# Performance work log

Hardware: AMD Instinct MI355X
Metric: run time of the kernel (lower is better)

## Reference

```python
import jax, jax.numpy as jnp
import numpy as np

NA, NT, NG = 100000, 300000, 2000        # artist / track / genre node counts
EPT, ETG = 600000, 400000                # performed / has_genre edge counts
IN_A, IN_T, IN_G = 64, 96, 32            # raw feature dims per node type
HID, HEADS, OUT, L = 64, 4, 64, 2        # GATv2 per-head dim = HID, concat=False
NEG_SLOPE = 0.2                          # GATv2 LeakyReLU slope


def setup_inputs() -> dict:
    key = jax.random.key(0)
    ks = jax.random.split(key, 32)
    f = lambda k, s, sc: jax.random.normal(k, s, dtype=jnp.float32) * sc
    z = lambda s: jnp.zeros(s, dtype=jnp.float32)
    return {
        "x_artist": f(ks[0], (NA, IN_A), 1.0),
        "x_track": f(ks[1], (NT, IN_T), 1.0),
        "x_genre": f(ks[2], (NG, IN_G), 1.0),
        "enc_Wa": f(ks[3], (IN_A, HID), 0.05), "enc_ba": z((HID,)),
        "enc_Wt": f(ks[4], (IN_T, HID), 0.05), "enc_bt": z((HID,)),
        "enc_Wg": f(ks[5], (IN_G, HID), 0.05), "enc_bg": z((HID,)),
        "src_pt": jax.random.randint(ks[6], (EPT,), 0, NA, dtype=jnp.int32),
        "dst_pt": jax.random.randint(ks[7], (EPT,), 0, NT, dtype=jnp.int32),
        "src_tg": jax.random.randint(ks[8], (ETG,), 0, NT, dtype=jnp.int32),
        "dst_tg": jax.random.randint(ks[9], (ETG,), 0, NG, dtype=jnp.int32),
        "Wl_pt": f(ks[10], (L, HID, HEADS, HID), 0.05), "bl_pt": z((L, HEADS, HID)),
        "Wr_pt": f(ks[11], (L, HID, HEADS, HID), 0.05), "br_pt": z((L, HEADS, HID)),
        "att_pt": f(ks[12], (L, HEADS, HID), 0.05), "bias_pt": z((L, HID)),
        "Wl_tg": f(ks[13], (L, HID, HEADS, HID), 0.05), "bl_tg": z((L, HEADS, HID)),
        "Wr_tg": f(ks[14], (L, HID, HEADS, HID), 0.05), "br_tg": z((L, HEADS, HID)),
        "att_tg": f(ks[15], (L, HEADS, HID), 0.05), "bias_tg": z((L, HID)),
        "lin_track_W": f(ks[16], (HID, OUT), 0.05), "lin_track_b": z((OUT,)),
        "lin_genre_W": f(ks[17], (HID, OUT), 0.05), "lin_genre_b": z((OUT,)),
    }


def _gatv2(xs, xd, src, dst, Wl, bl, Wr, br, att, bias, n_dst):
    """Bipartite GATv2Conv, heads averaged (concat=False), no self loops, eval mode."""
    gl = jnp.einsum("nd,dhc->nhc", xs, Wl) + bl            # [Ns,H,C] src transform
    gr = jnp.einsum("nd,dhc->nhc", xd, Wr) + br            # [Nd,H,C] dst transform
    e = jax.nn.leaky_relu(gl[src] + gr[dst], NEG_SLOPE)    # [E,H,C]
    s = jnp.einsum("ehc,hc->eh", e, att)                   # [E,H] logits
    m = jax.ops.segment_max(s, dst, num_segments=n_dst)    # per-dst softmax (stable)
    m = jnp.where(jnp.isfinite(m), m, 0.0)
    ex = jnp.exp(s - m[dst])
    den = jax.ops.segment_sum(ex, dst, num_segments=n_dst)
    alpha = ex / (den[dst] + 1e-16)                        # [E,H]
    out = jax.ops.segment_sum(gl[src] * alpha[:, :, None], dst, num_segments=n_dst)
    return out.mean(axis=1) + bias                         # [Nd,C]


def _l2norm(x):
    n = jnp.sqrt(jnp.sum(x * x, axis=-1, keepdims=True))
    return x / jnp.maximum(n, 1e-12)


def reference(x_artist, x_track, x_genre, enc_Wa, enc_ba, enc_Wt, enc_bt, enc_Wg, enc_bg,
              src_pt, dst_pt, src_tg, dst_tg,
              Wl_pt, bl_pt, Wr_pt, br_pt, att_pt, bias_pt,
              Wl_tg, bl_tg, Wr_tg, br_tg, att_tg, bias_tg,
              lin_track_W, lin_track_b, lin_genre_W, lin_genre_b):
    enc_a = x_artist @ enc_Wa + enc_ba
    enc_t = x_track @ enc_Wt + enc_bt
    enc_g = x_genre @ enc_Wg + enc_bg
    # Faithful to source: every layer reads the encoder output (hidden never fed back),
    # so only the last layer's weights determine the result.
    for l in range(L):
        h_track = jax.nn.elu(_gatv2(enc_a, enc_t, src_pt, dst_pt,
                                    Wl_pt[l], bl_pt[l], Wr_pt[l], br_pt[l],
                                    att_pt[l], bias_pt[l], NT))
        h_genre = jax.nn.elu(_gatv2(enc_t, enc_g, src_tg, dst_tg,
                                    Wl_tg[l], bl_tg[l], Wr_tg[l], br_tg[l],
                                    att_tg[l], bias_tg[l], NG))
    out_track = _l2norm(h_track @ lin_track_W + lin_track_b)
    out_genre = _l2norm(h_genre @ lin_genre_W + lin_genre_b)
    return out_track, out_genre
```

## Files before the change

kernel.cpp:

```cpp
#include <hip/hip_runtime.h>
#include <hip/hip_bf16.h>

typedef __hip_bfloat16 bf16;
typedef __attribute__((ext_vector_type(8))) short short8;
typedef __attribute__((ext_vector_type(4))) float f32x4;

#define NA 100000
#define NT 300000
#define NG 2000
#define EPT 600000
#define ETG 400000

#define DSB 64
#define DBK 64

#define DPP_QX1 0xB1
#define DPP_QX2 0x4E
#define DPP_RR4 0x124
#define DPP_RR8 0x128

template <int CTRL>
__device__ __forceinline__ float dppadd(float x) {
    int y = __builtin_amdgcn_update_dpp(0, __float_as_int(x), CTRL, 0xf, 0xf, true);
    return x + __int_as_float(y);
}

__device__ __forceinline__ float b2f(short s) {
    return __uint_as_float(((unsigned)(unsigned short)s) << 16);
}
__device__ __forceinline__ void cvt16(short8 a, short8 b, float* f) {
#pragma unroll
    for (int j = 0; j < 8; ++j) f[j] = b2f(a[j]);
#pragma unroll
    for (int j = 0; j < 8; ++j) f[8 + j] = b2f(b[j]);
}
__device__ __forceinline__ short f2bs(float x) {
    return (short)__builtin_bit_cast(unsigned short, __float2bfloat16(x));
}

__global__ void fill_u32(unsigned* __restrict__ p, unsigned v, long n) {
    long i = (long)blockIdx.x * 256 + threadIdx.x;
    if (i < n) p[i] = v;
}

__global__ __launch_bounds__(256) void wprep(
    const float* __restrict__ We, const float* __restrict__ Wl,
    const float* __restrict__ bl, const float* __restrict__ be,
    short* __restrict__ Bf, float* __restrict__ bc, int KS)
{
    int t = blockIdx.x * 256 + threadIdx.x;
    if (t < KS * 1024) {
        int c = t & 15, kb = (t >> 4) & 3, nt = (t >> 6) & 15, ks = t >> 10;
        int k0 = ks * 32 + kb * 8, n = nt * 16 + c;
        short8 o;
#pragma unroll
        for (int j = 0; j < 8; ++j) {
            int k = k0 + j;
            float acc = 0.f;
            for (int cc = 0; cc < 64; ++cc)
                acc = fmaf(We[k * 64 + cc], Wl[cc * 256 + n], acc);
            o[j] = f2bs(acc);
        }
        ((short8*)Bf)[t] = o;
    }
    if (blockIdx.x == 0) {
        int j = threadIdx.x;
        float acc = bl[j];
        for (int cc = 0; cc < 64; ++cc) acc = fmaf(be[cc], Wl[cc * 256 + j], acc);
        bc[j] = acc;
    }
}

template <int KS>
__global__ __launch_bounds__(256) void tformf(
    const float* __restrict__ A, const short* __restrict__ Bf,
    const float* __restrict__ bias, bf16* __restrict__ C, int M)
{
    constexpr int K = KS * 32;
    int wv = threadIdx.x >> 6, lane = threadIdx.x & 63;
    int lrow = lane & 15, kb = lane >> 4;
    int base = blockIdx.x * 64 + wv * 16;

    int arow = base + lrow; if (arow >= M) arow = M - 1;
    const float* Ap = A + (size_t)arow * K + kb * 8;
    short8 a[KS];
#pragma unroll
    for (int s = 0; s < KS; ++s) {
        f32x4 lo = *(const f32x4*)(Ap + s * 32);
        f32x4 hi = *(const f32x4*)(Ap + s * 32 + 4);
#pragma unroll
        for (int j = 0; j < 4; ++j) {
            a[s][j]     = f2bs(lo[j]);
            a[s][4 + j] = f2bs(hi[j]);
        }
    }

    const short8* Bl = (const short8*)Bf + kb * 16 + lrow;

    f32x4 acc[16];
#pragma unroll
    for (int nt = 0; nt < 16; ++nt) {
        float bv = bias[nt * 16 + lrow];
        f32x4 bvv = {bv, bv, bv, bv};
        acc[nt] = bvv;
    }
#pragma unroll
    for (int nt = 0; nt < 16; ++nt) {
#pragma unroll
        for (int s = 0; s < KS; ++s)
            acc[nt] = __builtin_amdgcn_mfma_f32_16x16x32_bf16(
                a[s], Bl[(s * 16 + nt) * 64], acc[nt], 0, 0, 0);
    }
    int r0 = base + kb * 4;
#pragma unroll
    for (int nt = 0; nt < 16; ++nt) {
#pragma unroll
        for (int r = 0; r < 4; ++r) {
            int row = r0 + r;
            if (row < M)
                C[(size_t)row * 256 + nt * 16 + lrow] = __float2bfloat16(acc[nt][r]);
        }
    }
}

__global__ __launch_bounds__(256) void histo(
    const int* __restrict__ dst, unsigned* __restrict__ cnt, int base, int E)
{
    int i = blockIdx.x * 256 + threadIdx.x;
    if (i < E) atomicAdd(&cnt[base + dst[i]], 1u);
}

__global__ __launch_bounds__(256) void scan_a(
    const unsigned* __restrict__ in, unsigned* __restrict__ out,
    unsigned* __restrict__ part, int n)
{
    __shared__ unsigned ts[256];
    int t = threadIdx.x;
    long base = (long)blockIdx.x * 1024 + (long)t * 4;
    unsigned v0 = 0, v1 = 0, v2 = 0, v3 = 0;
    if (base + 0 < n) v0 = in[base + 0];
    if (base + 1 < n) v1 = in[base + 1];
    if (base + 2 < n) v2 = in[base + 2];
    if (base + 3 < n) v3 = in[base + 3];
    unsigned s = v0 + v1 + v2 + v3;
    ts[t] = s;
    __syncthreads();
    unsigned run = s;
    for (int off = 1; off < 256; off <<= 1) {
        unsigned y = (t >= off) ? ts[t - off] : 0u;
        __syncthreads();
        run += y; ts[t] = run;
        __syncthreads();
    }
    unsigned ex = run - s;
    if (base + 0 < n) out[base + 0] = ex;
    if (base + 1 < n) out[base + 1] = ex + v0;
    if (base + 2 < n) out[base + 2] = ex + v0 + v1;
    if (base + 3 < n) out[base + 3] = ex + v0 + v1 + v2;
    if (t == 255) part[blockIdx.x] = run;
}

__global__ __launch_bounds__(256) void scan_c(
    unsigned* __restrict__ rp, const unsigned* __restrict__ part,
    unsigned* __restrict__ cur, int n)
{
    long i = (long)blockIdx.x * 256 + threadIdx.x;
    if (i >= n) return;
    unsigned v = rp[i] + part[i >> 10];
    rp[i] = v;
    if (i < n - 1) cur[i] = v;
}

__global__ __launch_bounds__(256) void scat(
    const int* __restrict__ src, const int* __restrict__ dst,
    unsigned* __restrict__ cur, int base, int* __restrict__ ss, int E)
{
    int i = blockIdx.x * 256 + threadIdx.x;
    if (i < E) {
        unsigned p = atomicAdd(&cur[base + dst[i]], 1u);
        ss[p] = src[i];
    }
}

__global__ __launch_bounds__(256) void deg_cnt(
    const unsigned* __restrict__ rp, unsigned* __restrict__ bcnt, int n)
{
    __shared__ unsigned hcnt[DBK];
    int b = blockIdx.x;
    int chunk = (n + DSB - 1) / DSB;
    int lo = b * chunk, hi = min(n, lo + chunk);
    if (threadIdx.x < DBK) hcnt[threadIdx.x] = 0u;
    __syncthreads();
    for (int i = lo + threadIdx.x; i < hi; i += 256) {
        unsigned deg = rp[i + 1] - rp[i];
        if (deg > DBK - 1) deg = DBK - 1;
        atomicAdd(&hcnt[deg], 1u);
    }
    __syncthreads();
    if (threadIdx.x < DBK) bcnt[(size_t)threadIdx.x * DSB + b] = hcnt[threadIdx.x];
}

__global__ __launch_bounds__(256) void scan4k(
    const unsigned* __restrict__ in, unsigned* __restrict__ out)
{
    __shared__ unsigned ts[256];
    int t = threadIdx.x;
    unsigned v[16]; unsigned s = 0;
#pragma unroll
    for (int j = 0; j < 16; ++j) { v[j] = in[t * 16 + j]; s += v[j]; }
    ts[t] = s;
    __syncthreads();
    unsigned run = s;
    for (int off = 1; off < 256; off <<= 1) {
        unsigned y = (t >= off) ? ts[t - off] : 0u;
        __syncthreads();
        run += y; ts[t] = run;
        __syncthreads();
    }
    unsigned ex = run - s;
#pragma unroll
    for (int j = 0; j < 16; ++j) { out[t * 16 + j] = ex; ex += v[j]; }
}

__global__ __launch_bounds__(256) void deg_place(
    const unsigned* __restrict__ rp, const unsigned* __restrict__ base,
    int* __restrict__ order, int n)
{
    __shared__ unsigned hcur[DBK];
    int b = blockIdx.x;
    int chunk = (n + DSB - 1) / DSB;
    int lo = b * chunk, hi = min(n, lo + chunk);
    if (threadIdx.x < DBK) hcur[threadIdx.x] = base[(size_t)threadIdx.x * DSB + b];
    __syncthreads();
    for (int i = lo + threadIdx.x; i < hi; i += 256) {
        unsigned deg = rp[i + 1] - rp[i];
        if (deg > DBK - 1) deg = DBK - 1;
        unsigned p = atomicAdd(&hcur[deg], 1u);
        order[p] = i;
    }
}

__global__ __launch_bounds__(256) void gat_w(
    const bf16* __restrict__ gl, const bf16* __restrict__ gr,
    const int* __restrict__ ssrc, const unsigned* __restrict__ rp,
    const int* __restrict__ order,
    const float* __restrict__ att, const float* __restrict__ bias,
    const float* __restrict__ linW, const float* __restrict__ linb,
    float* __restrict__ outp, int Nd)
{
    __shared__ float WL[4096];
    __shared__ float bL[64];
    __shared__ float hC[64];
    __shared__ float hL[16][68];
    for (int t = threadIdx.x; t < 4096; t += 256) WL[t] = linW[t];
    if (threadIdx.x < 64) {
        float b = bias[threadIdx.x];
        bL[threadIdx.x] = b;
        hC[threadIdx.x] = b > 0.f ? b : (__expf(b) - 1.f);
    }
    __syncthreads();

    int grp = threadIdx.x >> 4, g = threadIdx.x & 15;
    int h = g & 3, q = g >> 2;
    int eoff = h * 64 + q * 16;

    float at[16];
#pragma unroll
    for (int j = 0; j < 16; ++j) at[j] = att[eoff + j];
    f32x4 lbv = *(const f32x4*)(linb + g * 4);

    f32x4 ycn;
    {
        float y0 = lbv[0], y1 = lbv[1], y2 = lbv[2], y3 = lbv[3];
#pragma unroll
        for (int c = 0; c < 64; c += 4) {
            f32x4 hv = *(const f32x4*)&hC[c];
            const float* wr = WL + c * 64 + g * 4;
            f32x4 w0 = *(const f32x4*)(wr);
            f32x4 w1 = *(const f32x4*)(wr + 64);
            f32x4 w2 = *(const f32x4*)(wr + 128);
            f32x4 w3 = *(const f32x4*)(wr + 192);
            y0 = fmaf(hv[0], w0[0], y0); y1 = fmaf(hv[0], w0[1], y1);
            y2 = fmaf(hv[0], w0[2], y2); y3 = fmaf(hv[0], w0[3], y3);
            y0 = fmaf(hv[1], w1[0], y0); y1 = fmaf(hv[1], w1[1], y1);
            y2 = fmaf(hv[1], w1[2], y2); y3 = fmaf(hv[1], w1[3], y3);
            y0 = fmaf(hv[2], w2[0], y0); y1 = fmaf(hv[2], w2[1], y1);
            y2 = fmaf(hv[2], w2[2], y2); y3 = fmaf(hv[2], w2[3], y3);
            y0 = fmaf(hv[3], w3[0], y0); y1 = fmaf(hv[3], w3[1], y1);
            y2 = fmaf(hv[3], w3[2], y2); y3 = fmaf(hv[3], w3[3], y3);
        }
        float ss = y0 * y0 + y1 * y1 + y2 * y2 + y3 * y3;
        ss = dppadd<DPP_QX1>(ss);
        ss = dppadd<DPP_QX2>(ss);
        ss = dppadd<DPP_RR4>(ss);
        ss = dppadd<DPP_RR8>(ss);
        float rn = 1.f / fmaxf(sqrtf(ss), 1e-12f);
        ycn[0] = y0 * rn; ycn[1] = y1 * rn; ycn[2] = y2 * rn; ycn[3] = y3 * rn;
    }

    long ngroups = (Nd + 15) >> 4;
    for (long it = blockIdx.x; it < ngroups; it += gridDim.x) {
        long idx = it * 16 + grp;
        if (idx >= Nd) continue;
        int d = order[idx];
        unsigned beg = rp[d], end = rp[d + 1];
        if (beg == end) {
            *(f32x4*)(outp + (size_t)d * 64 + g * 4) = ycn;
            continue;
        }
        const short* grow = (const short*)gr + (size_t)d * 256 + eoff;
        short8 gr0 = *(const short8*)grow;
        short8 gr1 = *(const short8*)(grow + 8);
        float grf[16];
        cvt16(gr0, gr1, grf);

        float den = 0.f;
        float acc[16];
#pragma unroll
        for (int j = 0; j < 16; ++j) acc[j] = 0.f;

        unsigned e = beg;
        {
            int si = ssrc[e];
            const short* p0 = (const short*)gl + (size_t)si * 256 + eoff;
            short8 gA = *(const short8*)p0;
            short8 gB = *(const short8*)(p0 + 8);
            while (true) {
                float glf[16];
                cvt16(gA, gB, glf);
                ++e;
                bool more = e < end;
                if (more) {
                    int s2 = ssrc[e];
                    const short* p2 = (const short*)gl + (size_t)s2 * 256 + eoff;
                    gA = *(const short8*)p2;
                    gB = *(const short8*)(p2 + 8);
                }
                float pd = 0.f;
#pragma unroll
                for (int j = 0; j < 16; ++j) {
                    float v = glf[j] + grf[j];
                    float lr = fmaxf(v, 0.2f * v);
                    pd = fmaf(lr, at[j], pd);
                }
                pd = dppadd<DPP_RR4>(pd);
                pd = dppadd<DPP_RR8>(pd);
                float w = __expf(pd);
                den += w;
#pragma unroll
                for (int j = 0; j < 16; ++j) acc[j] = fmaf(w, glf[j], acc[j]);
                if (!more) break;
            }
        }
        float inv = 1.f / den;

        float x[16];
#pragma unroll
        for (int j = 0; j < 16; ++j) {
            float v = acc[j] * inv;
            v = dppadd<DPP_QX1>(v);
            v = dppadd<DPP_QX2>(v);
            x[j] = v;
        }
#pragma unroll
        for (int j = 0; j < 16; ++j) {
            float v = fmaf(0.25f, x[j], bL[q * 16 + j]);
            x[j] = v > 0.f ? v : (__expf(v) - 1.f);
        }
        if (h == 0) {
#pragma unroll
            for (int j = 0; j < 16; ++j) hL[grp][q * 16 + j] = x[j];
        }
        __builtin_amdgcn_wave_barrier();

        float y0 = lbv[0], y1 = lbv[1], y2 = lbv[2], y3 = lbv[3];
#pragma unroll
        for (int c = 0; c < 64; c += 4) {
            f32x4 hv = *(const f32x4*)&hL[grp][c];
            const float* wr = WL + c * 64 + g * 4;
            f32x4 w0 = *(const f32x4*)(wr);
            f32x4 w1 = *(const f32x4*)(wr + 64);
            f32x4 w2 = *(const f32x4*)(wr + 128);
            f32x4 w3 = *(const f32x4*)(wr + 192);
            y0 = fmaf(hv[0], w0[0], y0); y1 = fmaf(hv[0], w0[1], y1);
            y2 = fmaf(hv[0], w0[2], y2); y3 = fmaf(hv[0], w0[3], y3);
            y0 = fmaf(hv[1], w1[0], y0); y1 = fmaf(hv[1], w1[1], y1);
            y2 = fmaf(hv[1], w1[2], y2); y3 = fmaf(hv[1], w1[3], y3);
            y0 = fmaf(hv[2], w2[0], y0); y1 = fmaf(hv[2], w2[1], y1);
            y2 = fmaf(hv[2], w2[2], y2); y3 = fmaf(hv[2], w2[3], y3);
            y0 = fmaf(hv[3], w3[0], y0); y1 = fmaf(hv[3], w3[1], y1);
            y2 = fmaf(hv[3], w3[2], y2); y3 = fmaf(hv[3], w3[3], y3);
        }
        float ss = y0 * y0 + y1 * y1 + y2 * y2 + y3 * y3;
        ss = dppadd<DPP_QX1>(ss);
        ss = dppadd<DPP_QX2>(ss);
        ss = dppadd<DPP_RR4>(ss);
        ss = dppadd<DPP_RR8>(ss);
        float rn = 1.f / fmaxf(sqrtf(ss), 1e-12f);
        f32x4 yo = {y0 * rn, y1 * rn, y2 * rn, y3 * rn};
        *(f32x4*)(outp + (size_t)d * 64 + g * 4) = yo;
    }
}

__global__ __launch_bounds__(256) void gat_b(
    const bf16* __restrict__ gl, const bf16* __restrict__ gr,
    const int* __restrict__ ssrc, const unsigned* __restrict__ rp,
    const float* __restrict__ att, const float* __restrict__ bias,
    const float* __restrict__ linW, const float* __restrict__ linb,
    float* __restrict__ outp, int Nd)
{
    __shared__ float accL[16][256];
    __shared__ float denL[16][4];
    int grp = threadIdx.x >> 4, g = threadIdx.x & 15;
    int h = g & 3, q = g >> 2;
    int eoff = h * 64 + q * 16;
    int d = blockIdx.x;

    float at[16];
#pragma unroll
    for (int j = 0; j < 16; ++j) at[j] = att[eoff + j];

    const short* grow = (const short*)gr + (size_t)d * 256 + eoff;
    short8 gr0 = *(const short8*)grow;
    short8 gr1 = *(const short8*)(grow + 8);
    float grf[16];
    cvt16(gr0, gr1, grf);

    unsigned beg = rp[d], end = rp[d + 1];
    float den = 0.f;
    float acc[16];
#pragma unroll
    for (int j = 0; j < 16; ++j) acc[j] = 0.f;

    unsigned e = beg + grp;
    if (e < end) {
        int si = ssrc[e];
        const short* p0 = (const short*)gl + (size_t)si * 256 + eoff;
        short8 gA = *(const short8*)p0;
        short8 gB = *(const short8*)(p0 + 8);
        while (true) {
            float glf[16];
            cvt16(gA, gB, glf);
            e += 16;
            bool more = e < end;
            if (more) {
                int s2 = ssrc[e];
                const short* p2 = (const short*)gl + (size_t)s2 * 256 + eoff;
                gA = *(const short8*)p2;
                gB = *(const short8*)(p2 + 8);
            }
            float pd = 0.f;
#pragma unroll
            for (int j = 0; j < 16; ++j) {
                float v = glf[j] + grf[j];
                float lr = fmaxf(v, 0.2f * v);
                pd = fmaf(lr, at[j], pd);
            }
            pd = dppadd<DPP_RR4>(pd);
            pd = dppadd<DPP_RR8>(pd);
            float w = __expf(pd);
            den += w;
#pragma unroll
            for (int j = 0; j < 16; ++j) acc[j] = fmaf(w, glf[j], acc[j]);
            if (!more) break;
        }
    }
#pragma unroll
    for (int j = 0; j < 16; ++j) accL[grp][eoff + j] = acc[j];
    if (q == 0) denL[grp][h] = den;
    __syncthreads();

    int t = threadIdx.x;
    int hh = t >> 6, cc = t & 63;
    float sa = 0.f, sd = 0.f;
#pragma unroll
    for (int k = 0; k < 16; ++k) { sa += accL[k][hh * 64 + cc]; sd += denL[k][hh]; }
    float xv = sd > 0.f ? sa / sd : 0.f;
    __syncthreads();
    accL[0][t] = xv;
    __syncthreads();
    if (t < 64) {
        float m4 = 0.25f * (accL[0][t] + accL[0][64 + t] + accL[0][128 + t] + accL[0][192 + t]);
        float v = m4 + bias[t];
        accL[1][t] = v > 0.f ? v : (__expf(v) - 1.f);
    }
    __syncthreads();
    if (t < 64) {
        float y = linb[t];
        for (int c = 0; c < 64; ++c) y = fmaf(accL[1][c], linW[c * 64 + t], y);
        float ss = y * y;
        ss += __shfl_xor(ss, 1);  ss += __shfl_xor(ss, 2);  ss += __shfl_xor(ss, 4);
        ss += __shfl_xor(ss, 8);  ss += __shfl_xor(ss, 16); ss += __shfl_xor(ss, 32);
        float rn = 1.f / fmaxf(sqrtf(ss), 1e-12f);
        outp[(size_t)d * 64 + t] = y * rn;
    }
}


static inline unsigned gridFor(long n) { return (unsigned)((n + 255) / 256); }

extern "C" void kernel_launch(void* const* d_in, const int* in_sizes, int n_in,
                              void* d_out, int out_size, void* d_ws, size_t ws_size,
                              hipStream_t stream) {
    const float* x_artist = (const float*)d_in[0];
    const float* x_track  = (const float*)d_in[1];
    const float* x_genre  = (const float*)d_in[2];
    const float* enc_Wa = (const float*)d_in[3];  const float* enc_ba = (const float*)d_in[4];
    const float* enc_Wt = (const float*)d_in[5];  const float* enc_bt = (const float*)d_in[6];
    const float* enc_Wg = (const float*)d_in[7];  const float* enc_bg = (const float*)d_in[8];
    const int* src_pt = (const int*)d_in[9];
    const int* dst_pt = (const int*)d_in[10];
    const int* src_tg = (const int*)d_in[11];
    const int* dst_tg = (const int*)d_in[12];
    const float* Wl_pt   = (const float*)d_in[13] + 64 * 256;
    const float* bl_pt   = (const float*)d_in[14] + 256;
    const float* Wr_pt   = (const float*)d_in[15] + 64 * 256;
    const float* br_pt   = (const float*)d_in[16] + 256;
    const float* att_pt  = (const float*)d_in[17] + 256;
    const float* bias_pt = (const float*)d_in[18] + 64;
    const float* Wl_tg   = (const float*)d_in[19] + 64 * 256;
    const float* bl_tg   = (const float*)d_in[20] + 256;
    const float* Wr_tg   = (const float*)d_in[21] + 64 * 256;
    const float* br_tg   = (const float*)d_in[22] + 256;
    const float* att_tg  = (const float*)d_in[23] + 256;
    const float* bias_tg = (const float*)d_in[24] + 64;
    const float* lin_track_W = (const float*)d_in[25];
    const float* lin_track_b = (const float*)d_in[26];
    const float* lin_genre_W = (const float*)d_in[27];
    const float* lin_genre_b = (const float*)d_in[28];

    float* out = (float*)d_out;

    const int NTOT = NT + NG;

    char* p = (char*)d_ws;
    auto take = [&](size_t bytes) { char* q = p; p += (bytes + 255) & ~(size_t)255; return q; };
    char* region = take((size_t)NA * 256 * 2 + (size_t)NT * 256 * 2);
    bf16*  gl_pt  = (bf16*)region;
    bf16*  gr_pt  = (bf16*)(region + (size_t)NA * 256 * 2);
    bf16*  gl_tg  = (bf16*)region;
    unsigned* counts = (unsigned*)take((size_t)(NTOT + 1) * 4);
    unsigned* rowptr = (unsigned*)take((size_t)(NTOT + 1) * 4);
    unsigned* cursor = (unsigned*)take((size_t)NTOT * 4);
    unsigned* part   = (unsigned*)take((size_t)2048 * 4);
    int*      ssrc   = (int*)take((size_t)(EPT + ETG) * 4);
    int*      order  = (int*)take((size_t)NT * 4);
    unsigned* bcnt   = (unsigned*)take((size_t)DBK * DSB * 4);
    unsigned* bbase  = (unsigned*)take((size_t)DBK * DSB * 4);
    bf16*     gr_tg  = (bf16*)take((size_t)NG * 256 * 2);
    short*    Bf     = (short*)take((size_t)(64 + 96 + 96 + 32) * 256 * 2);
    float*    bc     = (float*)take((size_t)4 * 256 * 4);

    short* BfGLpt = Bf;
    short* BfGRpt = BfGLpt + 64 * 256;
    short* BfGLtg = BfGRpt + 96 * 256;
    short* BfGRtg = BfGLtg + 96 * 256;
    float* bcGLpt = bc;
    float* bcGRpt = bc + 256;
    float* bcGLtg = bc + 512;
    float* bcGRtg = bc + 768;

    dim3 blk(256);

    wprep<<<8,  blk, 0, stream>>>(enc_Wa, Wl_pt, bl_pt, enc_ba, BfGLpt, bcGLpt, 2);
    wprep<<<12, blk, 0, stream>>>(enc_Wt, Wr_pt, br_pt, enc_bt, BfGRpt, bcGRpt, 3);
    wprep<<<12, blk, 0, stream>>>(enc_Wt, Wl_tg, bl_tg, enc_bt, BfGLtg, bcGLtg, 3);
    wprep<<<4,  blk, 0, stream>>>(enc_Wg, Wr_tg, br_tg, enc_bg, BfGRtg, bcGRtg, 1);

    {
        int n = NTOT + 1;
        unsigned sgrid = (unsigned)((n + 1023) / 1024);
        fill_u32<<<gridFor(n), blk, 0, stream>>>(counts, 0u, n);
        histo<<<gridFor(EPT), blk, 0, stream>>>(dst_pt, counts, 0, EPT);
        histo<<<gridFor(ETG), blk, 0, stream>>>(dst_tg, counts, NT, ETG);
        scan_a<<<sgrid, blk, 0, stream>>>(counts, rowptr, part, n);
        scan_a<<<1, blk, 0, stream>>>(part, part, part + 1536, (int)sgrid);
        scan_c<<<gridFor(n), blk, 0, stream>>>(rowptr, part, cursor, n);
        scat<<<gridFor(EPT), blk, 0, stream>>>(src_pt, dst_pt, cursor, 0, ssrc, EPT);
        scat<<<gridFor(ETG), blk, 0, stream>>>(src_tg, dst_tg, cursor, NT, ssrc, ETG);
    }

    deg_cnt  <<<DSB, blk, 0, stream>>>(rowptr, bcnt, NT);
    scan4k   <<<1,   blk, 0, stream>>>(bcnt, bbase);
    deg_place<<<DSB, blk, 0, stream>>>(rowptr, bbase, order, NT);

    tformf<2><<<(NA + 63) / 64, blk, 0, stream>>>(x_artist, BfGLpt, bcGLpt, gl_pt, NA);
    tformf<3><<<(NT + 63) / 64, blk, 0, stream>>>(x_track,  BfGRpt, bcGRpt, gr_pt, NT);

    gat_w<<<2048, blk, 0, stream>>>(gl_pt, gr_pt, ssrc, rowptr, order, att_pt, bias_pt,
                                    lin_track_W, lin_track_b, out, NT);

    tformf<3><<<(NT + 63) / 64, blk, 0, stream>>>(x_track, BfGLtg, bcGLtg, gl_tg, NT);
    tformf<1><<<(NG + 63) / 64, blk, 0, stream>>>(x_genre, BfGRtg, bcGRtg, gr_tg, NG);

    gat_b<<<NG, blk, 0, stream>>>(gl_tg, gr_tg, ssrc, rowptr + NT, att_tg, bias_tg,
                                  lin_genre_W, lin_genre_b, out + (size_t)NT * 64, NG);
}
```

Measured before the change: 864.0 us.

## Permute GEMM output columns for vector stores and unroll edge loop by two

The weight-prep and bias indexing are permuted so that each lane holds 16 contiguous output columns. The GEMM epilogue can then pack bf16 pairs and write two 16-byte vector stores per row instead of 64 scalar 2-byte stores. The per-destination edge aggregation loop is rewritten to handle one odd edge and then process edges two at a time with independent gathers, which exposes more memory-level parallelism than the earlier one-ahead prefetch. The cost is higher register pressure, and the correctness of the column permutation depends on how the consumers interpret the layout.

```diff
diff --git a/kernel.cpp b/kernel.cpp
--- a/kernel.cpp
+++ b/kernel.cpp
@@ -4,6 +4,7 @@
 typedef __hip_bfloat16 bf16;
 typedef __attribute__((ext_vector_type(8))) short short8;
 typedef __attribute__((ext_vector_type(4))) float f32x4;
+typedef __attribute__((ext_vector_type(4))) unsigned u32x4;
 
 #define NA 100000
 #define NT 300000
@@ -51,7 +52,7 @@
     int t = blockIdx.x * 256 + threadIdx.x;
     if (t < KS * 1024) {
         int c = t & 15, kb = (t >> 4) & 3, nt = (t >> 6) & 15, ks = t >> 10;
-        int k0 = ks * 32 + kb * 8, n = nt * 16 + c;
+        int k0 = ks * 32 + kb * 8, n = c * 16 + nt;
         short8 o;
 #pragma unroll
         for (int j = 0; j < 8; ++j) {
@@ -100,7 +101,7 @@
     f32x4 acc[16];
 #pragma unroll
     for (int nt = 0; nt < 16; ++nt) {
-        float bv = bias[nt * 16 + lrow];
+        float bv = bias[lrow * 16 + nt];
         f32x4 bvv = {bv, bv, bv, bv};
         acc[nt] = bvv;
     }
@@ -113,13 +114,21 @@
     }
     int r0 = base + kb * 4;
 #pragma unroll
-    for (int nt = 0; nt < 16; ++nt) {
-#pragma unroll
-        for (int r = 0; r < 4; ++r) {
-            int row = r0 + r;
-            if (row < M)
-                C[(size_t)row * 256 + nt * 16 + lrow] = __float2bfloat16(acc[nt][r]);
-        }
+    for (int r = 0; r < 4; ++r) {
+        int row = r0 + r;
+        if (row >= M) continue;
+        unsigned w[8];
+#pragma unroll
+        for (int n4 = 0; n4 < 8; ++n4) {
+            unsigned lo = (unsigned)(unsigned short)f2bs(acc[2 * n4][r]);
+            unsigned hi = (unsigned)(unsigned short)f2bs(acc[2 * n4 + 1][r]);
+            w[n4] = lo | (hi << 16);
+        }
+        u32x4 v0 = {w[0], w[1], w[2], w[3]};
+        u32x4 v1 = {w[4], w[5], w[6], w[7]};
+        u32x4* dst = (u32x4*)(C + (size_t)row * 256 + lrow * 16);
+        dst[0] = v0;
+        dst[1] = v1;
     }
 }
 
@@ -320,37 +329,55 @@
         for (int j = 0; j < 16; ++j) acc[j] = 0.f;
 
         unsigned e = beg;
-        {
+        if ((end - beg) & 1u) {
             int si = ssrc[e];
             const short* p0 = (const short*)gl + (size_t)si * 256 + eoff;
             short8 gA = *(const short8*)p0;
             short8 gB = *(const short8*)(p0 + 8);
-            while (true) {
-                float glf[16];
-                cvt16(gA, gB, glf);
-                ++e;
-                bool more = e < end;
-                if (more) {
-                    int s2 = ssrc[e];
-                    const short* p2 = (const short*)gl + (size_t)s2 * 256 + eoff;
-                    gA = *(const short8*)p2;
-                    gB = *(const short8*)(p2 + 8);
-                }
-                float pd = 0.f;
-#pragma unroll
-                for (int j = 0; j < 16; ++j) {
-                    float v = glf[j] + grf[j];
-                    float lr = fmaxf(v, 0.2f * v);
-                    pd = fmaf(lr, at[j], pd);
-                }
-                pd = dppadd<DPP_RR4>(pd);
-                pd = dppadd<DPP_RR8>(pd);
-                float w = __expf(pd);
-                den += w;
-#pragma unroll
-                for (int j = 0; j < 16; ++j) acc[j] = fmaf(w, glf[j], acc[j]);
-                if (!more) break;
+            float glf[16];
+            cvt16(gA, gB, glf);
+            float pd = 0.f;
+#pragma unroll
+            for (int j = 0; j < 16; ++j) {
+                float v = glf[j] + grf[j];
+                pd = fmaf(fmaxf(v, 0.2f * v), at[j], pd);
             }
+            pd = dppadd<DPP_RR4>(pd);
+            pd = dppadd<DPP_RR8>(pd);
+            float w = __expf(pd);
+            den += w;
+#pragma unroll
+            for (int j = 0; j < 16; ++j) acc[j] = fmaf(w, glf[j], acc[j]);
+            ++e;
+        }
+        for (; e < end; e += 2) {
+            int s0 = ssrc[e], s1 = ssrc[e + 1];
+            const short* p0 = (const short*)gl + (size_t)s0 * 256 + eoff;
+            const short* p1 = (const short*)gl + (size_t)s1 * 256 + eoff;
+            short8 a0 = *(const short8*)p0;
+            short8 b0 = *(const short8*)(p0 + 8);
+            short8 a1 = *(const short8*)p1;
+            short8 b1 = *(const short8*)(p1 + 8);
+            float f0[16], f1[16];
+            cvt16(a0, b0, f0);
+            cvt16(a1, b1, f1);
+            float pd0 = 0.f, pd1 = 0.f;
+#pragma unroll
+            for (int j = 0; j < 16; ++j) {
+                float v0 = f0[j] + grf[j];
+                pd0 = fmaf(fmaxf(v0, 0.2f * v0), at[j], pd0);
+                float v1 = f1[j] + grf[j];
+                pd1 = fmaf(fmaxf(v1, 0.2f * v1), at[j], pd1);
+            }
+            pd0 = dppadd<DPP_RR4>(pd0);
+            pd0 = dppadd<DPP_RR8>(pd0);
+            pd1 = dppadd<DPP_RR4>(pd1);
+            pd1 = dppadd<DPP_RR8>(pd1);
+            float w0 = __expf(pd0), w1 = __expf(pd1);
+            den += w0 + w1;
+#pragma unroll
+            for (int j = 0; j < 16; ++j)
+                acc[j] = fmaf(w1, f1[j], fmaf(w0, f0[j], acc[j]));
         }
         float inv = 1.f / den;
 
```

New measurement: 998.0 us. 15.5% more time.
